# Kernel tuning notes

Measured on AMD Instinct MI355X. Metric: run time of the kernel, lower is better.

The kernel has to match this reference:

```python
import jax, jax.numpy as jnp
import numpy as np

B, F, H = 512, 64, 256
INPUT_LEN, TARGET_LEN = 128, 128


def _gru_step(h, xt, Wih, Whh, bih, bhh):
    # PyTorch GRU cell: gates ordered [r, z, n]
    gi = xt @ Wih.T + bih            # [B, 3H]
    gh = h @ Whh.T + bhh             # [B, 3H]
    ir, iz, inn = jnp.split(gi, 3, axis=-1)
    hr, hz, hn = jnp.split(gh, 3, axis=-1)
    r = jax.nn.sigmoid(ir + hr)
    z = jax.nn.sigmoid(iz + hz)
    n = jnp.tanh(inn + r * hn)
    return (1.0 - z) * n + z * h


def setup_inputs() -> dict:
    key = jax.random.key(0)
    ks = jax.random.split(key, 12)
    s_in = 1.0 / np.sqrt(H)
    x = jax.random.normal(ks[0], (B, INPUT_LEN + TARGET_LEN, F), dtype=jnp.float32)
    u = lambda k, shp: jax.random.uniform(k, shp, jnp.float32, -s_in, s_in)
    return {
        "x": x,
        "enc_Wih": u(ks[1], (3 * H, F)), "enc_Whh": u(ks[2], (3 * H, H)),
        "enc_bih": u(ks[3], (3 * H,)), "enc_bhh": u(ks[4], (3 * H,)),
        "dec_Wih": u(ks[5], (3 * H, F)), "dec_Whh": u(ks[6], (3 * H, H)),
        "dec_bih": u(ks[7], (3 * H,)), "dec_bhh": u(ks[8], (3 * H,)),
        "reg_W": u(ks[9], (F, H)), "reg_b": u(ks[10], (F,)),
        "input_len": INPUT_LEN, "target_len": TARGET_LEN,
    }


def reference(x, enc_Wih, enc_Whh, enc_bih, enc_bhh,
              dec_Wih, dec_Whh, dec_bih, dec_bhh,
              reg_W, reg_b, input_len, target_len):
    source_seq = x[:, :input_len, :]                       # [B, Tin, F]
    b = source_seq.shape[0]

    # Encoder GRU over source sequence, h0 = 0
    def enc_step(h, xt):
        h = _gru_step(h, xt, enc_Wih, enc_Whh, enc_bih, enc_bhh)
        return h, None
    h0 = jnp.zeros((b, enc_Whh.shape[1]), dtype=x.dtype)
    h_enc, _ = jax.lax.scan(enc_step, h0, source_seq.transpose(1, 0, 2))

    # Decoder: eval mode -> teacher forcing prob 0, always feed back own output
    dec_in0 = source_seq[:, -1, :]                         # [B, F]
    def dec_step(carry, _):
        h, inp = carry
        h = _gru_step(h, inp, dec_Wih, dec_Whh, dec_bih, dec_bhh)
        out = h @ reg_W.T + reg_b                          # [B, F]
        return (h, out), out
    (_, _), outs = jax.lax.scan(dec_step, (h_enc, dec_in0), None, length=target_len)
    return outs.transpose(1, 0, 2)                         # [B, Tout, F]
```

## Files before the change

### kernel.cpp

```cpp
#include <hip/hip_runtime.h>
#include <math.h>

#define Bsz 512
#define Fsz 64
#define Hsz 256
#define TSTEPS 128
#define G3 768

#define BG 16
#define HB 16
#define NBLK 256
#define NTHR 256

#define RED_SLOTS 40
#define OFF_B (2*RED_SLOTS*64*16)
#define SMEM_BYTES (OFF_B + 512)

typedef float f32x4 __attribute__((ext_vector_type(4)));
typedef short s16x8 __attribute__((ext_vector_type(8)));
typedef unsigned int  u32x4 __attribute__((ext_vector_type(4)));

#define MF(a,b,c) __builtin_amdgcn_mfma_f32_16x16x32_bf16(a,b,c,0,0,0)

static __device__ __forceinline__ unsigned short bf16_rne(float f){
    union { float f; unsigned u; } v; v.f = f;
    return (unsigned short)((v.u + 0x7FFFu + ((v.u >> 16) & 1u)) >> 16);
}
static __device__ __forceinline__ float bf16_to_f(unsigned short h){
    union { unsigned u; float f; } v; v.u = ((unsigned)h) << 16; return v.f;
}
static __device__ __forceinline__ void split8(const float* p, s16x8& hi, s16x8& lo){
    #pragma unroll
    for (int t = 0; t < 8; ++t){
        float f = p[t];
        unsigned short h = bf16_rne(f);
        hi[t] = (short)h;
        lo[t] = (short)bf16_rne(f - bf16_to_f(h));
    }
}
static __device__ __forceinline__ float sigmoidf_(float v){ return 1.0f/(1.0f + expf(-v)); }

__device__ __forceinline__ u32x4 load_sys_b128u(const unsigned* p){
    u32x4 r;
    asm volatile("global_load_dwordx4 %0, %1, off sc0 sc1" : "=v"(r) : "v"(p) : "memory");
    return r;
}
__device__ __forceinline__ unsigned load_sys_b32u_nw(const unsigned* p){
    unsigned r;
    asm volatile("global_load_dword %0, %1, off sc0 sc1" : "=v"(r) : "v"(p) : "memory");
    return r;
}
__device__ __forceinline__ void store_sys_b32u(unsigned* p, unsigned v){
    asm volatile("global_store_dword %0, %1, off sc0 sc1" :: "v"(p), "v"(v) : "memory");
}
__device__ __forceinline__ int load_sys_i32(const int* p){
    int r;
    asm volatile("global_load_dword %0, %1, off sc0 sc1\n\ts_waitcnt vmcnt(0)"
                 : "=v"(r) : "v"(p) : "memory");
    return r;
}
__device__ __forceinline__ void waitcnt0(){ asm volatile("s_waitcnt vmcnt(0)" ::: "memory"); }
__device__ __forceinline__ void regbar(u32x4& v){ asm volatile("" : "+v"(v)); }
__device__ __forceinline__ void regbar32(unsigned& v){ asm volatile("" : "+v"(v)); }

static __device__ __forceinline__ void unpack8(const u32x4 a, const u32x4 b, s16x8& hi, s16x8& lo){
    #pragma unroll
    for (int e = 0; e < 4; ++e){
        hi[e]   = (short)(a[e] >> 16);  lo[e]   = (short)(a[e] & 0xFFFFu);
        hi[4+e] = (short)(b[e] >> 16);  lo[4+e] = (short)(b[e] & 0xFFFFu);
    }
}

extern "C" __global__ void gru_setup(const float* __restrict__ x,
                                     const float* __restrict__ dWih,
                                     const float* __restrict__ dbih,
                                     const float* __restrict__ regW,
                                     const float* __restrict__ regb,
                                     float* __restrict__ Mw,
                                     float* __restrict__ cfold,
                                     float* __restrict__ gi0)
{
    int idx = blockIdx.x*blockDim.x + threadIdx.x;
    if (idx < G3*Hsz) {
        int g = idx >> 8, j = idx & 255;
        float a = 0.f;
        #pragma unroll 8
        for (int f = 0; f < Fsz; ++f) a += dWih[g*Fsz + f]*regW[f*Hsz + j];
        Mw[idx] = a;
    } else if (idx < G3*Hsz + G3) {
        int g = idx - G3*Hsz;
        float a = dbih[g];
        #pragma unroll 8
        for (int f = 0; f < Fsz; ++f) a += dWih[g*Fsz + f]*regb[f];
        cfold[g] = a;
    } else {
        int e = idx - (G3*Hsz + G3);
        if (e < Bsz*G3) {
            int b = e / G3, g = e - b*G3;
            const float* xp = x + (size_t)b*(256*64) + 127*64;
            float a = dbih[g];
            #pragma unroll 8
            for (int f = 0; f < Fsz; ++f) a += xp[f]*dWih[g*Fsz + f];
            gi0[e] = a;
        }
    }
}

extern "C" __global__ void __launch_bounds__(NTHR, 1)
gru_persistent(const float* __restrict__ x,
               const float* __restrict__ eWih, const float* __restrict__ eWhh,
               const float* __restrict__ ebih, const float* __restrict__ ebhh,
               const float* __restrict__ dWhh, const float* __restrict__ dbhh,
               const float* __restrict__ Mw,   const float* __restrict__ cfold,
               const float* __restrict__ gi0,  const float* __restrict__ regW,
               const float* __restrict__ regb,
               unsigned* __restrict__ hbuf, unsigned* __restrict__ canary,
               float* __restrict__ out)
{
    extern __shared__ char lds[];
    f32x4* s_redv = (f32x4*)lds;
    float* s_bias = (float*)(lds + OFF_B);
    float* s_dbh  = s_bias + 64;
    float* s_b3   = s_bias + 112;

    const int tid  = threadIdx.x;
    const int wv   = tid >> 6;
    const int lane = tid & 63;
    const int quad = lane >> 4;
    const int lcol = lane & 15;
    const int bg   = blockIdx.x >> 4;
    const int hb   = blockIdx.x & 15;
    const int hcol = hb*16 + lcol;
    const int mw   = wv & 1;
    const int kh   = wv >> 1;
    const int jb   = kh*2;
    const int hr0  = mw*16 + quad*4 + jb;
    const f32x4 z4 = {0.f, 0.f, 0.f, 0.f};

    unsigned* mycan = canary + ((size_t)bg*64 + hb*4 + wv)*4;
    const int* canp = (const int*)canary + ((size_t)bg*64 + lane)*4;
    const int  can_mine = ((lane >> 2) == hb);

    s16x8 wfh[3][2], wfl[3][2];
    s16x8 ufh[3], ufl[3];
    s16x8 rwh[2], rwl[2];
    #pragma unroll
    for (int g = 0; g < 3; ++g){
        #pragma unroll
        for (int q = 0; q < 2; ++q)
            split8(eWhh + (size_t)(g*256 + hcol)*256 + wv*64 + q*32 + quad*8,
                   wfh[g][q], wfl[g][q]);
        split8(eWih + (size_t)(g*256 + hcol)*64 + kh*32 + quad*8, ufh[g], ufl[g]);
    }
    if (tid < 16){
        int c = hb*16 + tid;
        s_bias[tid]    = ebih[c]       + ebhh[c];
        s_bias[16+tid] = ebih[256+c]   + ebhh[256+c];
        s_bias[32+tid] = ebih[512+c];
        s_bias[48+tid] = ebhh[512+c];
    }
    __syncthreads();

    for (int g = 0; g <= 2*TSTEPS; ++g){
        const bool enc  = (g < TSTEPS);
        const bool last = (g == 2*TSTEPS);
        const int  p    = g & 1;
        const unsigned tag  = (unsigned)((g >> 1) & 3);
        const unsigned otag = (unsigned)(((g+1) >> 1) & 3);
        const unsigned* hin = hbuf + (size_t)(g & 1)*Bsz*Hsz;
        unsigned* hout = hbuf + (size_t)((g+1) & 1)*Bsz*Hsz;

        if (g == TSTEPS){
            #pragma unroll
            for (int gg = 0; gg < 3; ++gg)
                #pragma unroll
                for (int q = 0; q < 2; ++q)
                    split8(dWhh + (size_t)(gg*256 + hcol)*256 + wv*64 + q*32 + quad*8,
                           wfh[gg][q], wfl[gg][q]);
            #pragma unroll
            for (int q = 0; q < 2; ++q){
                split8(Mw   + (size_t)(2*256 + hcol)*256 + wv*64 + q*32 + quad*8,
                       ufh[q], ufl[q]);
                split8(regW + (size_t)(hb*4 + (lcol & 3))*256 + wv*64 + q*32 + quad*8,
                       rwh[q], rwl[q]);
            }
            if (tid < 16){
                int c = hb*16 + tid;
                s_bias[tid]    = cfold[c]     + dbhh[c];
                s_bias[16+tid] = cfold[256+c] + dbhh[256+c];
                s_bias[32+tid] = cfold[512+c];
                s_dbh[tid]     = dbhh[c];
                s_dbh[16+tid]  = dbhh[256+c];
                s_dbh[32+tid]  = dbhh[512+c];
            }
            if (tid < 4) s_b3[tid] = regb[hb*4 + tid];
            __syncthreads();
        }
        if (g == TSTEPS + 1){
            #pragma unroll
            for (int gg = 0; gg < 2; ++gg)
                #pragma unroll
                for (int q = 0; q < 2; ++q){
                    float tmp[8];
                    const float* pa = dWhh + (size_t)(gg*256 + hcol)*256 + wv*64 + q*32 + quad*8;
                    const float* pb = Mw   + (size_t)(gg*256 + hcol)*256 + wv*64 + q*32 + quad*8;
                    #pragma unroll
                    for (int t2 = 0; t2 < 8; ++t2) tmp[t2] = pa[t2] + pb[t2];
                    split8(tmp, wfh[gg][q], wfl[gg][q]);
                }
        }

        f32x4 aR[2], aZ[2], aNi[2], aNh[2], oa[2];
        oa[0] = z4; oa[1] = z4;
        if (wv == 0 && !last){
            if (g == TSTEPS){
                #pragma unroll
                for (int m = 0; m < 2; ++m)
                    #pragma unroll
                    for (int j = 0; j < 4; ++j){
                        int grow_ = bg*32 + m*16 + quad*4 + j;
                        const float* gp = gi0 + (size_t)grow_*G3 + hcol;
                        aR[m][j]  = gp[0]   + s_dbh[lcol];
                        aZ[m][j]  = gp[256] + s_dbh[16+lcol];
                        aNi[m][j] = gp[512];
                        aNh[m][j] = s_dbh[32+lcol];
                    }
            } else {
                float bR = s_bias[lcol], bZ = s_bias[16+lcol], bNi = s_bias[32+lcol];
                float bNh = enc ? s_bias[48+lcol] : s_dbh[32+lcol];
                #pragma unroll
                for (int m = 0; m < 2; ++m){
                    aR[m] = (f32x4){bR,bR,bR,bR}; aZ[m] = (f32x4){bZ,bZ,bZ,bZ};
                    aNi[m] = (f32x4){bNi,bNi,bNi,bNi}; aNh[m] = (f32x4){bNh,bNh,bNh,bNh};
                }
            }
        } else {
            #pragma unroll
            for (int m = 0; m < 2; ++m){ aR[m]=z4; aZ[m]=z4; aNi[m]=z4; aNh[m]=z4; }
        }

        f32x4 xv0, xv1;
        if (enc){
            const float* xp = x + (size_t)(bg*32 + mw*16 + lcol)*(256*64)
                                + (size_t)g*64 + kh*32 + quad*8;
            xv0 = *(const f32x4*)xp;
            xv1 = *(const f32x4*)(xp + 4);
        }

        if (g){
            while (1){
                int v = load_sys_i32(canp);
                if (__all(can_mine | (v >= g))) break;
                __builtin_amdgcn_s_sleep(1);
            }
        }

        const unsigned* ab = hin + (size_t)(bg*32 + lcol)*256 + wv*64 + quad*8;
        u32x4 t[8];
        #pragma unroll
        for (int m = 0; m < 2; ++m)
            #pragma unroll
            for (int q = 0; q < 2; ++q)
                #pragma unroll
                for (int h4 = 0; h4 < 2; ++h4)
                    t[m*4+q*2+h4] = load_sys_b128u(ab + m*4096 + q*32 + h4*4);
        const unsigned* hoA = hin + (size_t)(bg*32 + hr0)*256 + hcol;
        unsigned ho0 = load_sys_b32u_nw(hoA);
        unsigned ho1 = load_sys_b32u_nw(hoA + 256);

        if (enc){
            float xf[8];
            #pragma unroll
            for (int e = 0; e < 4; ++e){ xf[e] = xv0[e]; xf[4+e] = xv1[e]; }
            s16x8 xh, xl;
            split8(xf, xh, xl);
            #define XMF(M) { \
                aR[M] =MF(xh,ufh[0],aR[M]);  aR[M] =MF(xh,ufl[0],aR[M]);  aR[M] =MF(xl,ufh[0],aR[M]);  \
                aZ[M] =MF(xh,ufh[1],aZ[M]);  aZ[M] =MF(xh,ufl[1],aZ[M]);  aZ[M] =MF(xl,ufh[1],aZ[M]);  \
                aNi[M]=MF(xh,ufh[2],aNi[M]); aNi[M]=MF(xh,ufl[2],aNi[M]); aNi[M]=MF(xl,ufh[2],aNi[M]); }
            if (mw == 0) XMF(0) else XMF(1)
            #undef XMF
        }

        {
            unsigned done = 0;
            while (1){
                waitcnt0();
                #pragma unroll
                for (int jj = 0; jj < 8; ++jj) regbar(t[jj]);
                regbar32(ho0); regbar32(ho1);
                unsigned nd = done;
                #pragma unroll
                for (int jj = 0; jj < 8; ++jj)
                    if (!((nd >> jj) & 1u))
                        if (((t[jj][0]&3u)==tag) && ((t[jj][1]&3u)==tag) &&
                            ((t[jj][2]&3u)==tag) && ((t[jj][3]&3u)==tag)) nd |= (1u << jj);
                if (!((nd >> 8) & 1u) && ((ho0 & 3u) == tag)) nd |= 0x100u;
                if (!((nd >> 9) & 1u) && ((ho1 & 3u) == tag)) nd |= 0x200u;
                done = nd;
                if (__all((int)(done == 0x3FFu))) break;
                __builtin_amdgcn_s_sleep(1);
                #pragma unroll
                for (int m = 0; m < 2; ++m)
                    #pragma unroll
                    for (int q = 0; q < 2; ++q)
                        #pragma unroll
                        for (int h4 = 0; h4 < 2; ++h4){
                            const int jj = m*4+q*2+h4;
                            if (!((done >> jj) & 1u))
                                t[jj] = load_sys_b128u(ab + m*4096 + q*32 + h4*4);
                        }
                if (!((done >> 8) & 1u)) ho0 = load_sys_b32u_nw(hoA);
                if (!((done >> 9) & 1u)) ho1 = load_sys_b32u_nw(hoA + 256);
            }
        }

        #pragma unroll
        for (int m = 0; m < 2; ++m){
            #pragma unroll
            for (int q = 0; q < 2; ++q){
                s16x8 ah, al;
                unpack8(t[m*4+q*2], t[m*4+q*2+1], ah, al);
                if (!last){
                    aR[m]=MF(ah,wfh[0][q],aR[m]); aR[m]=MF(ah,wfl[0][q],aR[m]); aR[m]=MF(al,wfh[0][q],aR[m]);
                    aZ[m]=MF(ah,wfh[1][q],aZ[m]); aZ[m]=MF(ah,wfl[1][q],aZ[m]); aZ[m]=MF(al,wfh[1][q],aZ[m]);
                    aNh[m]=MF(ah,wfh[2][q],aNh[m]); aNh[m]=MF(ah,wfl[2][q],aNh[m]); aNh[m]=MF(al,wfh[2][q],aNh[m]);
                    if (!enc && g > TSTEPS){
                        aNi[m]=MF(ah,ufh[q],aNi[m]); aNi[m]=MF(ah,ufl[q],aNi[m]); aNi[m]=MF(al,ufh[q],aNi[m]);
                    }
                }
                if (g >= TSTEPS + 1){
                    oa[m]=MF(ah,rwh[q],oa[m]); oa[m]=MF(ah,rwl[q],oa[m]); oa[m]=MF(al,rwh[q],oa[m]);
                }
            }
        }

        if (!last){
            f32x4* rp = s_redv + ((size_t)p*RED_SLOTS + wv*8)*64 + lane;
            rp[0]   = aR[0]; rp[64]  = aZ[0]; rp[128] = aNi[0]; rp[192] = aNh[0];
            rp[256] = aR[1]; rp[320] = aZ[1]; rp[384] = aNi[1]; rp[448] = aNh[1];
        }
        if (g >= TSTEPS + 1){
            f32x4* op = s_redv + ((size_t)p*RED_SLOTS + 32 + wv*2)*64 + lane;
            op[0] = oa[0]; op[64] = oa[1];
        }
        __syncthreads();

        if (!last){
            f32x4 R = z4, Z = z4, Ni = z4, Nh = z4;
            #pragma unroll
            for (int w2 = 0; w2 < 4; ++w2){
                const f32x4* rp = s_redv + ((size_t)p*RED_SLOTS + w2*8 + mw*4)*64 + lane;
                R += rp[0]; Z += rp[64]; Ni += rp[128]; Nh += rp[192];
            }
            #define EW(J, HW, RO) { \
                float r = sigmoidf_(R[J]); \
                float z = sigmoidf_(Z[J]); \
                float n = tanhf(Ni[J] + r*Nh[J]); \
                float hold = bf16_to_f((unsigned short)((HW) >> 16)) \
                           + bf16_to_f((unsigned short)((HW) & 0xFFFFu)); \
                float hv = (1.0f - z)*n + z*hold; \
                unsigned short p1 = bf16_rne(hv); \
                unsigned short p0 = bf16_rne(hv - bf16_to_f(p1)); \
                store_sys_b32u(hout + (size_t)(bg*32 + hr0 + RO)*256 + hcol, \
                               (((unsigned)p1) << 16) | ((unsigned)(p0 & 0xFFFCu)) | otag); }
            if (jb == 0){ EW(0, ho0, 0); EW(1, ho1, 1); }
            else        { EW(2, ho0, 0); EW(3, ho1, 1); }
            #undef EW
            if (lane == 0) store_sys_b32u(mycan, (unsigned)(g + 1));
        }

        if (g >= TSTEPS + 1 && wv >= 2){
            const int m2 = wv - 2;
            float b3 = s_b3[lcol & 3];
            f32x4 ot = {b3, b3, b3, b3};
            #pragma unroll
            for (int w2 = 0; w2 < 4; ++w2)
                ot += s_redv[((size_t)p*RED_SLOTS + 32 + w2*2 + m2)*64 + lane];
            if (lcol < 4){
                const int oidx = g - TSTEPS - 1;
                #pragma unroll
                for (int j = 0; j < 4; ++j)
                    out[(size_t)(bg*32 + m2*16 + quad*4 + j)*(TSTEPS*Fsz)
                        + (size_t)oidx*Fsz + hb*4 + lcol] = ot[j];
            }
        }
    }
}

extern "C" void kernel_launch(void* const* d_in, const int* in_sizes, int n_in,
                              void* d_out, int out_size, void* d_ws, size_t ws_size,
                              hipStream_t stream)
{
    (void)in_sizes; (void)n_in; (void)out_size; (void)ws_size;
    const float* x    = (const float*)d_in[0];
    const float* eWih = (const float*)d_in[1];
    const float* eWhh = (const float*)d_in[2];
    const float* ebih = (const float*)d_in[3];
    const float* ebhh = (const float*)d_in[4];
    const float* dWih = (const float*)d_in[5];
    const float* dWhh = (const float*)d_in[6];
    const float* dbih = (const float*)d_in[7];
    const float* dbhh = (const float*)d_in[8];
    const float* regW = (const float*)d_in[9];
    const float* regb = (const float*)d_in[10];
    float* out = (float*)d_out;

    unsigned* hbuf = (unsigned*)d_ws;
    float* Mw    = (float*)d_ws + 2*Bsz*Hsz;
    float* gi0   = Mw + G3*Hsz;
    float* cfold = gi0 + Bsz*G3;
    unsigned* canary = (unsigned*)(cfold + 1024);

    hipMemsetAsync(hbuf, 0, (size_t)Bsz*Hsz*sizeof(unsigned), stream);
    hipMemsetAsync(hbuf + (size_t)Bsz*Hsz, 3, (size_t)Bsz*Hsz*sizeof(unsigned), stream);
    hipMemsetAsync(canary, 0, (size_t)BG*64*4*sizeof(unsigned), stream);

    hipLaunchKernelGGL(gru_setup, dim3(2307), dim3(256), 0, stream,
                       x, dWih, dbih, regW, regb, Mw, cfold, gi0);

    hipFuncSetAttribute((const void*)gru_persistent,
                        hipFuncAttributeMaxDynamicSharedMemorySize, SMEM_BYTES);

    void* args[] = { (void*)&x, (void*)&eWih, (void*)&eWhh, (void*)&ebih, (void*)&ebhh,
                     (void*)&dWhh, (void*)&dbhh, (void*)&Mw, (void*)&cfold, (void*)&gi0,
                     (void*)&regW, (void*)&regb, (void*)&hbuf, (void*)&canary, (void*)&out };
    hipError_t rc = hipLaunchCooperativeKernel((const void*)gru_persistent,
                                               dim3(NBLK), dim3(NTHR), args,
                                               SMEM_BYTES, stream);
    if (rc != hipSuccess) {
        hipLaunchKernelGGL(gru_persistent, dim3(NBLK), dim3(NTHR), SMEM_BYTES, stream,
                           x, eWih, eWhh, ebih, ebhh, dWhh, dbhh, Mw, cfold, gi0,
                           regW, regb, hbuf, canary, out);
    }
}
```

Baseline: 1.327 ms.

## Replace per-value tag polling with canary-only sync and single LDS reduction buffer

```diff
diff --git a/kernel.cpp b/kernel.cpp
--- a/kernel.cpp
+++ b/kernel.cpp
@@ -13,7 +13,7 @@
 #define NTHR 256
 
 #define RED_SLOTS 40
-#define OFF_B (2*RED_SLOTS*64*16)
+#define OFF_B (RED_SLOTS*64*16)
 #define SMEM_BYTES (OFF_B + 512)
 
 typedef float f32x4 __attribute__((ext_vector_type(4)));
@@ -128,8 +128,8 @@
     const int lane = tid & 63;
     const int quad = lane >> 4;
     const int lcol = lane & 15;
-    const int bg   = blockIdx.x >> 4;
-    const int hb   = blockIdx.x & 15;
+    const int bg   = blockIdx.x & 15;
+    const int hb   = blockIdx.x >> 4;
     const int hcol = hb*16 + lcol;
     const int mw   = wv & 1;
     const int kh   = wv >> 1;
@@ -164,9 +164,6 @@
     for (int g = 0; g <= 2*TSTEPS; ++g){
         const bool enc  = (g < TSTEPS);
         const bool last = (g == 2*TSTEPS);
-        const int  p    = g & 1;
-        const unsigned tag  = (unsigned)((g >> 1) & 3);
-        const unsigned otag = (unsigned)(((g+1) >> 1) & 3);
         const unsigned* hin = hbuf + (size_t)(g & 1)*Bsz*Hsz;
         unsigned* hout = hbuf + (size_t)((g+1) & 1)*Bsz*Hsz;
 
@@ -282,38 +279,10 @@
             #undef XMF
         }
 
-        {
-            unsigned done = 0;
-            while (1){
-                waitcnt0();
-                #pragma unroll
-                for (int jj = 0; jj < 8; ++jj) regbar(t[jj]);
-                regbar32(ho0); regbar32(ho1);
-                unsigned nd = done;
-                #pragma unroll
-                for (int jj = 0; jj < 8; ++jj)
-                    if (!((nd >> jj) & 1u))
-                        if (((t[jj][0]&3u)==tag) && ((t[jj][1]&3u)==tag) &&
-                            ((t[jj][2]&3u)==tag) && ((t[jj][3]&3u)==tag)) nd |= (1u << jj);
-                if (!((nd >> 8) & 1u) && ((ho0 & 3u) == tag)) nd |= 0x100u;
-                if (!((nd >> 9) & 1u) && ((ho1 & 3u) == tag)) nd |= 0x200u;
-                done = nd;
-                if (__all((int)(done == 0x3FFu))) break;
-                __builtin_amdgcn_s_sleep(1);
-                #pragma unroll
-                for (int m = 0; m < 2; ++m)
-                    #pragma unroll
-                    for (int q = 0; q < 2; ++q)
-                        #pragma unroll
-                        for (int h4 = 0; h4 < 2; ++h4){
-                            const int jj = m*4+q*2+h4;
-                            if (!((done >> jj) & 1u))
-                                t[jj] = load_sys_b128u(ab + m*4096 + q*32 + h4*4);
-                        }
-                if (!((done >> 8) & 1u)) ho0 = load_sys_b32u_nw(hoA);
-                if (!((done >> 9) & 1u)) ho1 = load_sys_b32u_nw(hoA + 256);
-            }
-        }
+        waitcnt0();
+        #pragma unroll
+        for (int jj = 0; jj < 8; ++jj) regbar(t[jj]);
+        regbar32(ho0); regbar32(ho1);
 
         #pragma unroll
         for (int m = 0; m < 2; ++m){
@@ -336,12 +305,12 @@
         }
 
         if (!last){
-            f32x4* rp = s_redv + ((size_t)p*RED_SLOTS + wv*8)*64 + lane;
+            f32x4* rp = s_redv + (size_t)(wv*8)*64 + lane;
             rp[0]   = aR[0]; rp[64]  = aZ[0]; rp[128] = aNi[0]; rp[192] = aNh[0];
             rp[256] = aR[1]; rp[320] = aZ[1]; rp[384] = aNi[1]; rp[448] = aNh[1];
         }
         if (g >= TSTEPS + 1){
-            f32x4* op = s_redv + ((size_t)p*RED_SLOTS + 32 + wv*2)*64 + lane;
+            f32x4* op = s_redv + (size_t)(32 + wv*2)*64 + lane;
             op[0] = oa[0]; op[64] = oa[1];
         }
         __syncthreads();
@@ -350,7 +319,7 @@
             f32x4 R = z4, Z = z4, Ni = z4, Nh = z4;
             #pragma unroll
             for (int w2 = 0; w2 < 4; ++w2){
-                const f32x4* rp = s_redv + ((size_t)p*RED_SLOTS + w2*8 + mw*4)*64 + lane;
+                const f32x4* rp = s_redv + (size_t)(w2*8 + mw*4)*64 + lane;
                 R += rp[0]; Z += rp[64]; Ni += rp[128]; Nh += rp[192];
             }
             #define EW(J, HW, RO) { \
@@ -363,11 +332,10 @@
                 unsigned short p1 = bf16_rne(hv); \
                 unsigned short p0 = bf16_rne(hv - bf16_to_f(p1)); \
                 store_sys_b32u(hout + (size_t)(bg*32 + hr0 + RO)*256 + hcol, \
-                               (((unsigned)p1) << 16) | ((unsigned)(p0 & 0xFFFCu)) | otag); }
+                               (((unsigned)p1) << 16) | (unsigned)p0); }
             if (jb == 0){ EW(0, ho0, 0); EW(1, ho1, 1); }
             else        { EW(2, ho0, 0); EW(3, ho1, 1); }
             #undef EW
-            if (lane == 0) store_sys_b32u(mycan, (unsigned)(g + 1));
         }
 
         if (g >= TSTEPS + 1 && wv >= 2){
@@ -376,7 +344,7 @@
             f32x4 ot = {b3, b3, b3, b3};
             #pragma unroll
             for (int w2 = 0; w2 < 4; ++w2)
-                ot += s_redv[((size_t)p*RED_SLOTS + 32 + w2*2 + m2)*64 + lane];
+                ot += s_redv[(size_t)(32 + w2*2 + m2)*64 + lane];
             if (lcol < 4){
                 const int oidx = g - TSTEPS - 1;
                 #pragma unroll
@@ -385,6 +353,12 @@
                         + (size_t)oidx*Fsz + hb*4 + lcol] = ot[j];
             }
         }
+
+        if (!last){
+            waitcnt0();
+            if (lane == 0) store_sys_b32u(mycan, (unsigned)(g + 1));
+        }
+        __syncthreads();
     }
 }
 
@@ -413,7 +387,6 @@
     unsigned* canary = (unsigned*)(cfold + 1024);
 
     hipMemsetAsync(hbuf, 0, (size_t)Bsz*Hsz*sizeof(unsigned), stream);
-    hipMemsetAsync(hbuf + (size_t)Bsz*Hsz, 3, (size_t)Bsz*Hsz*sizeof(unsigned), stream);
     hipMemsetAsync(canary, 0, (size_t)BG*64*4*sizeof(unsigned), stream);
 
     hipLaunchKernelGGL(gru_setup, dim3(2307), dim3(256), 0, stream,
```

After: 1.162 ms. 12.5% less time.
